# Kernel optimization log

Measured on AMD Instinct MI355X. Metric: run time of the kernel, lower is better.

Reference implementation:

```python
import jax, jax.numpy as jnp
import numpy as np

D_MODEL = 1024
N_HEADS = 16
HEAD = D_MODEL // N_HEADS  # 64


def setup_inputs() -> dict:
    key = jax.random.key(0)
    ks = jax.random.split(key, 6)
    B, T = 2, 2048
    x = jax.random.normal(ks[0], (B, T, D_MODEL), dtype=jnp.float32)
    s_in = 1.0 / np.sqrt(HEAD)
    # per-head projections: Linear(head_size -> d_model), no bias. Stored as [H, head, d_model].
    Wq = jax.random.normal(ks[1], (N_HEADS, HEAD, D_MODEL), dtype=jnp.float32) * s_in
    Wk = jax.random.normal(ks[2], (N_HEADS, HEAD, D_MODEL), dtype=jnp.float32) * s_in
    Wv = jax.random.normal(ks[3], (N_HEADS, HEAD, D_MODEL), dtype=jnp.float32) * s_in
    # output projection: Linear(H*d_model -> d_model) with bias
    Wo = jax.random.normal(ks[4], (N_HEADS * D_MODEL, D_MODEL), dtype=jnp.float32) / np.sqrt(N_HEADS * D_MODEL)
    bo = jax.random.normal(ks[5], (D_MODEL,), dtype=jnp.float32) * 0.01
    return {"x": x, "Wq": Wq, "Wk": Wk, "Wv": Wv, "Wo": Wo, "bo": bo}


def reference(x, Wq, Wk, Wv, Wo, bo):
    B, T, _ = x.shape
    # split into per-head slices: [B, H, T, head]
    xh = x.reshape(B, T, N_HEADS, HEAD).transpose(0, 2, 1, 3)
    q = jnp.einsum("bhtd,hdm->bhtm", xh, Wq)  # [B,H,T,d_model]
    k = jnp.einsum("bhtd,hdm->bhtm", xh, Wk)
    v = jnp.einsum("bhtd,hdm->bhtm", xh, Wv)
    # scale uses D = head input dim (= HEAD), per the original code
    scores = jnp.einsum("bhtm,bhsm->bhts", q, k) / jnp.sqrt(jnp.asarray(HEAD, x.dtype))
    weights = jax.nn.softmax(scores, axis=-1)
    vb = jnp.einsum("bhts,bhsm->bhtm", weights, v)  # [B,H,T,d_model]
    cat = vb.transpose(0, 2, 1, 3).reshape(B, T, N_HEADS * D_MODEL)
    return cat @ Wo + bo
```

## Files before the change

kernel.cpp:

```cpp
#include <hip/hip_runtime.h>
#include <math.h>

typedef unsigned u32;
typedef unsigned short u16;
typedef __attribute__((ext_vector_type(8))) __bf16 bf16x8;
typedef __attribute__((ext_vector_type(4))) float f32x4;

#define DEVI __device__ __forceinline__

DEVI u16 f2bf(float f) {
    u32 u = __builtin_bit_cast(u32, f);
    u += 0x7fffu + ((u >> 16) & 1u);
    return (u16)(u >> 16);
}

DEVI u32 packbf(float a, float b) {
    u32 ua = __builtin_bit_cast(u32, a) + 0x8000u;
    u32 ub = __builtin_bit_cast(u32, b) + 0x8000u;
    return (ua >> 16) | (ub & 0xffff0000u);
}

DEVI bf16x8 ldsf(const u16* p) { return *(const bf16x8*)p; }

DEVI f32x4 mfma16(bf16x8 a, bf16x8 b, f32x4 c) {
    return __builtin_amdgcn_mfma_f32_16x16x32_bf16(a, b, c, 0, 0, 0);
}

#if __has_builtin(__builtin_amdgcn_exp2f)
DEVI float fexp2(float x) { return __builtin_amdgcn_exp2f(x); }
#else
DEVI float fexp2(float x) { return exp2f(x); }
#endif

__global__ __launch_bounds__(256) void k_pw(const float* __restrict__ x,
                                            const float* __restrict__ Wq, const float* __restrict__ Wk,
                                            const float* __restrict__ Wv, const float* __restrict__ Wo,
                                            u16* __restrict__ xswz, u16* __restrict__ xt2,
                                            u16* __restrict__ mtg, u16* __restrict__ W2) {
    __shared__ __align__(16) char SM[36864];
    const int tid = threadIdx.x;
    const int id = blockIdx.x;
    const int rr = tid >> 2, c16 = (tid & 3) * 16;

    if (id < 272) {
        u16* LA0 = (u16*)SM;
        u16* LB0 = (u16*)(SM + 9216);
        u16* LA1 = (u16*)(SM + 18432);
        u16* LB1 = (u16*)(SM + 27648);
        const int w = tid >> 6, lane = tid & 63, g = lane >> 4, ln = lane & 15;
        f32x4 acc[4] = {};
        float4 pa0[4], pb0[4], pa1[4], pb1[4];

        auto mm = [&](const u16* LAp, const u16* LBp) {
#pragma unroll
            for (int ks = 0; ks < 2; ks++) {
                bf16x8 bb = ldsf(LBp + (w * 16 + ln) * 72 + ks * 32 + g * 8);
#pragma unroll
                for (int mt = 0; mt < 4; mt++) {
                    bf16x8 a = ldsf(LAp + (mt * 16 + ln) * 72 + ks * 32 + g * 8);
                    acc[mt] = mfma16(a, bb, acc[mt]);
                }
            }
        };
        auto bar = [&]() {
            asm volatile("s_waitcnt lgkmcnt(0)" ::: "memory");
            __builtin_amdgcn_s_barrier();
            __builtin_amdgcn_sched_barrier(0);
        };

        if (id >= 256) {
            const int h = id - 256;
            auto loadT = [&](int t, float4* pa, float4* pb) {
                const float4* sa = (const float4*)(Wk + (h * 64 + rr) * 1024 + t * 64 + c16);
                const float4* sb = (const float4*)(Wq + (h * 64 + rr) * 1024 + t * 64 + c16);
#pragma unroll
                for (int j = 0; j < 4; j++) { pa[j] = sa[j]; pb[j] = sb[j]; }
            };
            auto cvtW = [&](u16* LAp, u16* LBp, float4* pa, float4* pb) {
                union { uint4 q[2]; u16 s[16]; } ua, ub;
#pragma unroll
                for (int j = 0; j < 4; j++) {
                    ua.s[j*4+0]=f2bf(pa[j].x); ua.s[j*4+1]=f2bf(pa[j].y); ua.s[j*4+2]=f2bf(pa[j].z); ua.s[j*4+3]=f2bf(pa[j].w);
                    ub.s[j*4+0]=f2bf(pb[j].x); ub.s[j*4+1]=f2bf(pb[j].y); ub.s[j*4+2]=f2bf(pb[j].z); ub.s[j*4+3]=f2bf(pb[j].w);
                }
                *(uint4*)(LAp + rr * 72 + c16) = ua.q[0]; *(uint4*)(LAp + rr * 72 + c16 + 8) = ua.q[1];
                *(uint4*)(LBp + rr * 72 + c16) = ub.q[0]; *(uint4*)(LBp + rr * 72 + c16 + 8) = ub.q[1];
            };
            loadT(0, pa0, pb0);
            cvtW(LA0, LB0, pa0, pb0);
            loadT(1, pa1, pb1);
            bar();
            for (int kb = 0; kb < 16; kb += 2) {
                if (kb + 2 < 16) loadT(kb + 2, pa0, pb0);
                mm(LA0, LB0);
                cvtW(LA1, LB1, pa1, pb1);
                bar();
                if (kb + 3 < 16) loadT(kb + 3, pa1, pb1);
                mm(LA1, LB1);
                if (kb + 2 < 16) cvtW(LA0, LB0, pa0, pb0);
                bar();
            }
#pragma unroll
            for (int mt = 0; mt < 4; mt++)
#pragma unroll
                for (int r = 0; r < 4; r++)
                    mtg[h * 4096 + (mt * 16 + g * 4 + r) * 64 + w * 16 + ln] =
                        f2bf(acc[mt][r] * 0.18033688011112f);
        } else {
            const int h = id >> 4, n0 = (id & 15) * 64;
            auto loadT = [&](int t, float4* pa, float4* pb) {
                const float4* sa = (const float4*)(Wo + (h * 1024 + t * 64 + rr) * 1024 + n0 + c16);
                const float4* sb = (const float4*)(Wv + (h * 64 + rr) * 1024 + t * 64 + c16);
#pragma unroll
                for (int j = 0; j < 4; j++) { pa[j] = sa[j]; pb[j] = sb[j]; }
            };
            auto cvtW = [&](u16* LAp, u16* LBp, float4* pa, float4* pb) {
                union { uint4 q[2]; u16 s[16]; } ub;
#pragma unroll
                for (int j = 0; j < 4; j++) {
                    ub.s[j*4+0]=f2bf(pb[j].x); ub.s[j*4+1]=f2bf(pb[j].y); ub.s[j*4+2]=f2bf(pb[j].z); ub.s[j*4+3]=f2bf(pb[j].w);
                }
                *(uint4*)(LBp + rr * 72 + c16) = ub.q[0]; *(uint4*)(LBp + rr * 72 + c16 + 8) = ub.q[1];
#pragma unroll
                for (int j = 0; j < 4; j++) {
                    LAp[(c16 + j * 4 + 0) * 72 + rr] = f2bf(pa[j].x);
                    LAp[(c16 + j * 4 + 1) * 72 + rr] = f2bf(pa[j].y);
                    LAp[(c16 + j * 4 + 2) * 72 + rr] = f2bf(pa[j].z);
                    LAp[(c16 + j * 4 + 3) * 72 + rr] = f2bf(pa[j].w);
                }
            };
            loadT(0, pa0, pb0);
            cvtW(LA0, LB0, pa0, pb0);
            loadT(1, pa1, pb1);
            bar();
            for (int kb = 0; kb < 16; kb += 2) {
                if (kb + 2 < 16) loadT(kb + 2, pa0, pb0);
                mm(LA0, LB0);
                cvtW(LA1, LB1, pa1, pb1);
                bar();
                if (kb + 3 < 16) loadT(kb + 3, pa1, pb1);
                mm(LA1, LB1);
                if (kb + 2 < 16) cvtW(LA0, LB0, pa0, pb0);
                bar();
            }
            int d = w * 16 + ln;
#pragma unroll
            for (int mt = 0; mt < 4; mt++)
#pragma unroll
                for (int r = 0; r < 4; r++) {
                    int n = n0 + mt * 16 + g * 4 + r;
                    W2[h * 65536 + n * 64 + (((d >> 3) ^ (n & 7)) << 3) + (d & 7)] = f2bf(acc[mt][r]);
                }
        }
    } else {
        const int pid = id - 272;
        const int kt = pid & 31, h = (pid >> 5) & 15, b = pid >> 9, bh = b * 16 + h;
        float* T = (float*)SM;
        int t = kt * 64 + rr;
        const float4* gx = (const float4*)(x + (b * 2048 + t) * 1024 + h * 64 + c16);
        float4 f[4];
#pragma unroll
        for (int j = 0; j < 4; j++) f[j] = gx[j];
#pragma unroll
        for (int j = 0; j < 4; j++) {
            T[rr * 65 + c16 + j * 4 + 0] = f[j].x; T[rr * 65 + c16 + j * 4 + 1] = f[j].y;
            T[rr * 65 + c16 + j * 4 + 2] = f[j].z; T[rr * 65 + c16 + j * 4 + 3] = f[j].w;
        }
        {
            union { uint4 q[2]; u16 s[16]; } u;
#pragma unroll
            for (int j = 0; j < 4; j++) {
                u.s[j * 4 + 0] = f2bf(f[j].x); u.s[j * 4 + 1] = f2bf(f[j].y);
                u.s[j * 4 + 2] = f2bf(f[j].z); u.s[j * 4 + 3] = f2bf(f[j].w);
            }
            u16* dst = xswz + (bh * 2048 + t) * 64;
            int c0 = (tid & 3) * 2, sw = rr & 7;
            *(uint4*)(dst + ((c0 ^ sw) << 3))       = u.q[0];
            *(uint4*)(dst + (((c0 + 1) ^ sw) << 3)) = u.q[1];
        }
        __syncthreads();
        int dd = tid >> 2, t4 = (tid & 3) * 16;
        union { uint2 d2[4]; u16 s[16]; } ou;
#pragma unroll
        for (int j = 0; j < 16; j++) ou.s[j] = f2bf(T[(t4 + j) * 65 + dd]);
        u16* dst = xt2 + bh * 131072 + kt * 4096 + dd * 64;
        const int nt0 = t4 >> 4;
        const int cb = (nt0 >> 1) * 4;
        const int off = (nt0 & 1) * 4;
        const int sw = dd & 7;
#pragma unroll
        for (int g4 = 0; g4 < 4; g4++) {
            int c = cb + g4;
            *(uint2*)(dst + ((c ^ sw) << 3) + off) = ou.d2[g4];
        }
    }
}

__global__ __launch_bounds__(256, 2) void k_attn(const u16* __restrict__ xswz, const u16* __restrict__ xt2,
                                                 const u16* __restrict__ mtg, u16* __restrict__ U2) {
    __shared__ __align__(16) u16 smem[16384];
    u16* KB = smem;

    const int tid = threadIdx.x;
    const int w = tid >> 6, lane = tid & 63, g = lane >> 4, ln = lane & 15, ln7 = lane & 7;
    const int nid = (blockIdx.x & 7) * 64 + (blockIdx.x >> 3);
    const int qt = nid & 15, h = (nid >> 4) & 15, b = nid >> 8, bh = b * 16 + h;
    const u16* xs = xswz + bh * 131072;
    const u16* xv = xt2 + bh * 131072;

    bf16x8 qf[2][2];
    {
        u16* LM  = smem;
        u16* LXQ = smem + 4608;
        {
            int r4 = tid >> 2, c4 = (tid & 3) * 2;
            const uint4* gm = (const uint4*)(mtg + h * 4096 + r4 * 64);
            uint4 m0 = gm[c4], m1 = gm[c4 + 1];
            *(uint4*)(LM + r4 * 72 + c4 * 8)     = m0;
            *(uint4*)(LM + r4 * 72 + c4 * 8 + 8) = m1;
            int r2 = tid >> 1, c2 = (tid & 1) * 4;
            const uint4* gx = (const uint4*)(xs + (qt * 128 + r2) * 64);
            uint4 x0 = gx[c2], x1 = gx[c2 + 1], x2 = gx[c2 + 2], x3 = gx[c2 + 3];
            *(uint4*)(LXQ + r2 * 72 + c2 * 8)      = x0;
            *(uint4*)(LXQ + r2 * 72 + c2 * 8 + 8)  = x1;
            *(uint4*)(LXQ + r2 * 72 + c2 * 8 + 16) = x2;
            *(uint4*)(LXQ + r2 * 72 + c2 * 8 + 24) = x3;
        }
        __syncthreads();
        f32x4 acc[2][4] = {};
#pragma unroll
        for (int qh = 0; qh < 2; qh++) {
            int row = qh * 64 + w * 16 + ln;
#pragma unroll
            for (int ks = 0; ks < 2; ks++) {
                bf16x8 a = ldsf(LXQ + row * 72 + (((ks * 4 + g) ^ ln7) << 3));
#pragma unroll
                for (int nt = 0; nt < 4; nt++) {
                    bf16x8 bb = ldsf(LM + (nt * 16 + ln) * 72 + ks * 32 + g * 8);
                    acc[qh][nt] = mfma16(a, bb, acc[qh][nt]);
                }
            }
        }
        __syncthreads();
#pragma unroll
        for (int qh = 0; qh < 2; qh++) {
            u16* QLw = smem + qh * 4608 + w * 1152;
#pragma unroll
            for (int nt = 0; nt < 4; nt++)
#pragma unroll
                for (int r = 0; r < 4; r++)
                    QLw[(g * 4 + r) * 72 + nt * 16 + ln] = f2bf(acc[qh][nt][r]);
        }
        asm volatile("s_waitcnt lgkmcnt(0)" ::: "memory");
#pragma unroll
        for (int qh = 0; qh < 2; qh++) {
            u16* QLw = smem + qh * 4608 + w * 1152;
            qf[qh][0] = ldsf(QLw + ln * 72 + g * 8);
            qf[qh][1] = ldsf(QLw + ln * 72 + 32 + g * 8);
        }
        __syncthreads();
    }

    {
        const uint4* gk = (const uint4*)xs;
        uint4 k0 = gk[tid], k1 = gk[tid + 256];
        uint4* lk = (uint4*)KB;
        lk[tid] = k0; lk[tid + 256] = k1;
    }
    bf16x8 vfA[2][4], vfB[2][4];
#pragma unroll
    for (int ks = 0; ks < 2; ks++)
#pragma unroll
        for (int dt = 0; dt < 4; dt++)
            vfA[ks][dt] = *(const bf16x8*)(xv + (dt * 16 + ln) * 64 + (((ks * 4 + g) ^ ln7) << 3));
    asm volatile("s_waitcnt lgkmcnt(0)" ::: "memory");
    __builtin_amdgcn_s_barrier();
    __builtin_amdgcn_sched_barrier(0);

    float lrow[2] = {0.f, 0.f};
    f32x4 o[2][4] = {};

    auto step = [&](int kt, bf16x8 (&vcur)[2][4], bf16x8 (&vnxt)[2][4]) {
        const int cur = (kt & 1) << 12;
        const u16* KL = KB + cur;
        uint4 kr0, kr1;
        if (kt + 1 < 32) {
            const uint4* gk = (const uint4*)(xs + (kt + 1) * 4096);
            kr0 = gk[tid]; kr1 = gk[tid + 256];
            const u16* gv = xv + (kt + 1) * 4096;
#pragma unroll
            for (int ks = 0; ks < 2; ks++)
#pragma unroll
                for (int dt = 0; dt < 4; dt++)
                    vnxt[ks][dt] = *(const bf16x8*)(gv + (dt * 16 + ln) * 64 + (((ks * 4 + g) ^ ln7) << 3));
        }

        f32x4 s[2][4] = {};
        __builtin_amdgcn_s_setprio(1);
#pragma unroll
        for (int ks = 0; ks < 2; ks++) {
#pragma unroll
            for (int nt = 0; nt < 4; nt++) {
                bf16x8 a = ldsf(KL + (nt * 16 + ln) * 64 + (((ks * 4 + g) ^ ln7) << 3));
                s[0][nt] = mfma16(a, qf[0][ks], s[0][nt]);
                s[1][nt] = mfma16(a, qf[1][ks], s[1][nt]);
            }
        }
        __builtin_amdgcn_s_setprio(0);

        u32 pk[2][4][2];
#pragma unroll
        for (int qh = 0; qh < 2; qh++) {
            float ts = 0.f;
#pragma unroll
            for (int nt = 0; nt < 4; nt++) {
                float p0 = fexp2(s[qh][nt][0]), p1 = fexp2(s[qh][nt][1]);
                float p2 = fexp2(s[qh][nt][2]), p3 = fexp2(s[qh][nt][3]);
                pk[qh][nt][0] = packbf(p0, p1);
                pk[qh][nt][1] = packbf(p2, p3);
                ts += (p0 + p1) + (p2 + p3);
            }
            lrow[qh] += ts;
        }

        __builtin_amdgcn_s_setprio(1);
#pragma unroll
        for (int ks = 0; ks < 2; ks++) {
            union { u32 u[4]; bf16x8 v; } pf[2];
#pragma unroll
            for (int qh = 0; qh < 2; qh++) {
                pf[qh].u[0] = pk[qh][2 * ks][0];
                pf[qh].u[1] = pk[qh][2 * ks][1];
                pf[qh].u[2] = pk[qh][2 * ks + 1][0];
                pf[qh].u[3] = pk[qh][2 * ks + 1][1];
            }
#pragma unroll
            for (int dt = 0; dt < 4; dt++) {
                o[0][dt] = mfma16(vcur[ks][dt], pf[0].v, o[0][dt]);
                o[1][dt] = mfma16(vcur[ks][dt], pf[1].v, o[1][dt]);
            }
        }
        __builtin_amdgcn_s_setprio(0);

        if (kt + 1 < 32) {
            const int nxt = cur ^ 4096;
            uint4* lk = (uint4*)(KB + nxt);
            lk[tid] = kr0; lk[tid + 256] = kr1;
        }
        asm volatile("s_waitcnt lgkmcnt(0)" ::: "memory");
        __builtin_amdgcn_s_barrier();
        __builtin_amdgcn_sched_barrier(0);
    };

    for (int kt = 0; kt < 32; kt += 2) {
        step(kt, vfA, vfB);
        step(kt + 1, vfB, vfA);
    }

#pragma unroll
    for (int qh = 0; qh < 2; qh++) {
        lrow[qh] += __shfl_xor(lrow[qh], 16, 64);
        lrow[qh] += __shfl_xor(lrow[qh], 32, 64);
        float inv = 1.0f / lrow[qh];
        int t = b * 2048 + qt * 128 + qh * 64 + w * 16 + ln;
#pragma unroll
        for (int dt = 0; dt < 4; dt++) {
            ushort4 vv;
            vv.x = f2bf(o[qh][dt][0] * inv); vv.y = f2bf(o[qh][dt][1] * inv);
            vv.z = f2bf(o[qh][dt][2] * inv); vv.w = f2bf(o[qh][dt][3] * inv);
            int c = dt * 2 + (g >> 1);
            int pos = c ^ (t & 7);
            *(ushort4*)(U2 + h * 262144 + t * 64 + pos * 8 + (g & 1) * 4) = vv;
        }
    }
}

__global__ __launch_bounds__(512) void k_out(const u16* __restrict__ U2, const u16* __restrict__ W2,
                                             const float* __restrict__ bo, float* __restrict__ out) {
    __shared__ __align__(16) u16 SMu[32768];
    const int tid = threadIdx.x;
    const int w = tid >> 6, lane = tid & 63, g = lane >> 4, ln = lane & 15;
    const int nid = (blockIdx.x & 7) * 32 + (blockIdx.x >> 3);
    const int n0 = (nid & 7) * 128, r0 = (nid >> 3) * 128;
    const int wr = (w >> 2) * 64, wc = (w & 3) * 32;
    f32x4 acc[4][2] = {};
    uint4 ar[2], br[2];

    {
        const uint4* ga = (const uint4*)(U2 + r0 * 64);
        const uint4* gb = (const uint4*)(W2 + n0 * 64);
        ar[0] = ga[tid]; ar[1] = ga[tid + 512];
        br[0] = gb[tid]; br[1] = gb[tid + 512];
        ((uint4*)SMu)[tid] = ar[0]; ((uint4*)SMu)[tid + 512] = ar[1];
        ((uint4*)(SMu + 16384))[tid] = br[0]; ((uint4*)(SMu + 16384))[tid + 512] = br[1];
    }
    asm volatile("s_waitcnt lgkmcnt(0)" ::: "memory");
    __builtin_amdgcn_s_barrier();
    __builtin_amdgcn_sched_barrier(0);

    for (int kb = 0; kb < 16; kb++) {
        const int cu = (kb & 1) << 13;
        if (kb + 1 < 16) {
            const uint4* ga = (const uint4*)(U2 + (kb + 1) * 262144 + r0 * 64);
            const uint4* gb = (const uint4*)(W2 + (kb + 1) * 65536 + n0 * 64);
            ar[0] = ga[tid]; ar[1] = ga[tid + 512];
            br[0] = gb[tid]; br[1] = gb[tid + 512];
        }
        const u16* AL = SMu + cu;
        const u16* BL = SMu + 16384 + cu;
#pragma unroll
        for (int ks = 0; ks < 2; ks++) {
            bf16x8 af[4], bfr[2];
#pragma unroll
            for (int mt = 0; mt < 4; mt++) {
                int rr = wr + mt * 16 + ln;
                af[mt] = ldsf(AL + rr * 64 + (((ks * 4 + g) ^ (rr & 7)) << 3));
            }
#pragma unroll
            for (int nt = 0; nt < 2; nt++) {
                int rr = wc + nt * 16 + ln;
                bfr[nt] = ldsf(BL + rr * 64 + (((ks * 4 + g) ^ (rr & 7)) << 3));
            }
#pragma unroll
            for (int mt = 0; mt < 4; mt++)
#pragma unroll
                for (int nt = 0; nt < 2; nt++)
                    acc[mt][nt] = mfma16(af[mt], bfr[nt], acc[mt][nt]);
        }
        if (kb + 1 < 16) {
            const int nx = cu ^ 8192;
            uint4* la = (uint4*)(SMu + nx);
            uint4* lb = (uint4*)(SMu + 16384 + nx);
            la[tid] = ar[0]; la[tid + 512] = ar[1];
            lb[tid] = br[0]; lb[tid + 512] = br[1];
        }
        asm volatile("s_waitcnt lgkmcnt(0)" ::: "memory");
        __builtin_amdgcn_s_barrier();
        __builtin_amdgcn_sched_barrier(0);
    }

    float* Wp = (float*)SMu + w * 576;
    const int coff = (lane & 7) * 4;
    const float4 b4 = *(const float4*)(bo + n0 + wc + coff);
#pragma unroll
    for (int mt = 0; mt < 4; mt++) {
#pragma unroll
        for (int nt = 0; nt < 2; nt++)
#pragma unroll
            for (int r = 0; r < 4; r++)
                Wp[(g * 4 + r) * 36 + nt * 16 + ln] = acc[mt][nt][r];
        asm volatile("s_waitcnt lgkmcnt(0)" ::: "memory");
#pragma unroll
        for (int i = 0; i < 2; i++) {
            int row = (lane >> 3) + 8 * i;
            float4 v = *(const float4*)(Wp + row * 36 + coff);
            v.x += b4.x; v.y += b4.y; v.z += b4.z; v.w += b4.w;
            *(float4*)(out + (r0 + wr + mt * 16 + row) * 1024 + n0 + wc + coff) = v;
        }
    }
}

extern "C" void kernel_launch(void* const* d_in, const int* in_sizes, int n_in,
                              void* d_out, int out_size, void* d_ws, size_t ws_size,
                              hipStream_t stream) {
    const float* x  = (const float*)d_in[0];
    const float* Wq = (const float*)d_in[1];
    const float* Wk = (const float*)d_in[2];
    const float* Wv = (const float*)d_in[3];
    const float* Wo = (const float*)d_in[4];
    const float* bo = (const float*)d_in[5];
    float* out = (float*)d_out;

    char* ws = (char*)d_ws;
    u16* xswz = (u16*)(ws);
    u16* mtg  = (u16*)(ws + 8388608);
    u16* xt2  = (u16*)(ws + 8519680);
    u16* W2   = (u16*)(ws + 16908288);
    u16* U2   = (u16*)(ws + 19005440);

    k_pw<<<1296, 256, 0, stream>>>(x, Wq, Wk, Wv, Wo, xswz, xt2, mtg, W2);
    k_attn<<<512, 256, 0, stream>>>(xswz, xt2, mtg, U2);
    k_out<<<256, 512, 0, stream>>>(U2, W2, bo, out);
}
```

Before: 207.8 us.

## Split KV tiles across waves and stage V in LDS with cross-wave reduction

Restructures the attention kernel so each wave handles 64 queries (4 q-tiles) against half of each 64-key tile, instead of 32 queries against the full tile. V is now double-buffered through LDS alongside K rather than loaded per-lane straight from global into registers. At the end, partial outputs and row sums from the two KV-half waves are combined through LDS before normalisation. The aim is more reuse of each K/V fragment across query tiles and coalesced V loads, at the cost of more accumulator registers, extra LDS, and a final reduction pass.

```diff
diff --git a/kernel.cpp b/kernel.cpp
--- a/kernel.cpp
+++ b/kernel.cpp
@@ -198,17 +198,19 @@
 
 __global__ __launch_bounds__(256, 2) void k_attn(const u16* __restrict__ xswz, const u16* __restrict__ xt2,
                                                  const u16* __restrict__ mtg, u16* __restrict__ U2) {
-    __shared__ __align__(16) u16 smem[16384];
+    __shared__ __align__(16) u16 smem[20480];
     u16* KB = smem;
+    u16* VB = smem + 8192;
 
     const int tid = threadIdx.x;
     const int w = tid >> 6, lane = tid & 63, g = lane >> 4, ln = lane & 15, ln7 = lane & 7;
+    const int kvh = w & 1, qh2 = w >> 1;
     const int nid = (blockIdx.x & 7) * 64 + (blockIdx.x >> 3);
-    const int qt = nid & 15, h = (nid >> 4) & 15, b = nid >> 8, bh = b * 16 + h;
+    const int qtb = nid & 15, h = (nid >> 4) & 15, b = nid >> 8, bh = b * 16 + h;
     const u16* xs = xswz + bh * 131072;
     const u16* xv = xt2 + bh * 131072;
 
-    bf16x8 qf[2][2];
+    bf16x8 qf[4][2];
     {
         u16* LM  = smem;
         u16* LXQ = smem + 4608;
@@ -219,7 +221,7 @@
             *(uint4*)(LM + r4 * 72 + c4 * 8)     = m0;
             *(uint4*)(LM + r4 * 72 + c4 * 8 + 8) = m1;
             int r2 = tid >> 1, c2 = (tid & 1) * 4;
-            const uint4* gx = (const uint4*)(xs + (qt * 128 + r2) * 64);
+            const uint4* gx = (const uint4*)(xs + (qtb * 128 + r2) * 64);
             uint4 x0 = gx[c2], x1 = gx[c2 + 1], x2 = gx[c2 + 2], x3 = gx[c2 + 3];
             *(uint4*)(LXQ + r2 * 72 + c2 * 8)      = x0;
             *(uint4*)(LXQ + r2 * 72 + c2 * 8 + 8)  = x1;
@@ -251,48 +253,42 @@
                 for (int r = 0; r < 4; r++)
                     QLw[(g * 4 + r) * 72 + nt * 16 + ln] = f2bf(acc[qh][nt][r]);
         }
-        asm volatile("s_waitcnt lgkmcnt(0)" ::: "memory");
-#pragma unroll
-        for (int qh = 0; qh < 2; qh++) {
-            u16* QLw = smem + qh * 4608 + w * 1152;
-            qf[qh][0] = ldsf(QLw + ln * 72 + g * 8);
-            qf[qh][1] = ldsf(QLw + ln * 72 + 32 + g * 8);
+        __syncthreads();
+#pragma unroll
+        for (int qt = 0; qt < 4; qt++) {
+            const u16* QLr = smem + qh2 * 4608 + qt * 1152;
+            qf[qt][0] = ldsf(QLr + ln * 72 + g * 8);
+            qf[qt][1] = ldsf(QLr + ln * 72 + 32 + g * 8);
         }
         __syncthreads();
     }
 
     {
         const uint4* gk = (const uint4*)xs;
-        uint4 k0 = gk[tid], k1 = gk[tid + 256];
+        const uint4* gv = (const uint4*)xv;
+        uint4 k0 = gk[tid], k1 = gk[tid + 256], v0 = gv[tid], v1 = gv[tid + 256];
         uint4* lk = (uint4*)KB;
-        lk[tid] = k0; lk[tid + 256] = k1;
-    }
-    bf16x8 vfA[2][4], vfB[2][4];
-#pragma unroll
-    for (int ks = 0; ks < 2; ks++)
-#pragma unroll
-        for (int dt = 0; dt < 4; dt++)
-            vfA[ks][dt] = *(const bf16x8*)(xv + (dt * 16 + ln) * 64 + (((ks * 4 + g) ^ ln7) << 3));
+        uint4* lv = (uint4*)VB;
+        lk[tid] = k0; lk[tid + 256] = k1; lv[tid] = v0; lv[tid + 256] = v1;
+    }
     asm volatile("s_waitcnt lgkmcnt(0)" ::: "memory");
     __builtin_amdgcn_s_barrier();
     __builtin_amdgcn_sched_barrier(0);
 
-    float lrow[2] = {0.f, 0.f};
-    f32x4 o[2][4] = {};
-
-    auto step = [&](int kt, bf16x8 (&vcur)[2][4], bf16x8 (&vnxt)[2][4]) {
+    float lrow[4] = {0.f, 0.f, 0.f, 0.f};
+    f32x4 o[4][4] = {};
+
+#pragma unroll 2
+    for (int kt = 0; kt < 32; ++kt) {
         const int cur = (kt & 1) << 12;
         const u16* KL = KB + cur;
-        uint4 kr0, kr1;
+        const u16* VL = VB + cur;
+
+        uint4 kr0, kr1, vr0, vr1;
         if (kt + 1 < 32) {
             const uint4* gk = (const uint4*)(xs + (kt + 1) * 4096);
-            kr0 = gk[tid]; kr1 = gk[tid + 256];
-            const u16* gv = xv + (kt + 1) * 4096;
-#pragma unroll
-            for (int ks = 0; ks < 2; ks++)
-#pragma unroll
-                for (int dt = 0; dt < 4; dt++)
-                    vnxt[ks][dt] = *(const bf16x8*)(gv + (dt * 16 + ln) * 64 + (((ks * 4 + g) ^ ln7) << 3));
+            const uint4* gv = (const uint4*)(xv + (kt + 1) * 4096);
+            kr0 = gk[tid]; kr1 = gk[tid + 256]; vr0 = gv[tid]; vr1 = gv[tid + 256];
         }
 
         f32x4 s[2][4] = {};
@@ -300,44 +296,46 @@
 #pragma unroll
         for (int ks = 0; ks < 2; ks++) {
 #pragma unroll
-            for (int nt = 0; nt < 4; nt++) {
-                bf16x8 a = ldsf(KL + (nt * 16 + ln) * 64 + (((ks * 4 + g) ^ ln7) << 3));
-                s[0][nt] = mfma16(a, qf[0][ks], s[0][nt]);
-                s[1][nt] = mfma16(a, qf[1][ks], s[1][nt]);
+            for (int nt = 0; nt < 2; nt++) {
+                bf16x8 a = ldsf(KL + ((kvh * 2 + nt) * 16 + ln) * 64 + (((ks * 4 + g) ^ ln7) << 3));
+#pragma unroll
+                for (int qt = 0; qt < 4; qt++)
+                    s[nt][qt] = mfma16(a, qf[qt][ks], s[nt][qt]);
             }
         }
         __builtin_amdgcn_s_setprio(0);
 
         u32 pk[2][4][2];
 #pragma unroll
-        for (int qh = 0; qh < 2; qh++) {
+        for (int qt = 0; qt < 4; qt++) {
             float ts = 0.f;
 #pragma unroll
-            for (int nt = 0; nt < 4; nt++) {
-                float p0 = fexp2(s[qh][nt][0]), p1 = fexp2(s[qh][nt][1]);
-                float p2 = fexp2(s[qh][nt][2]), p3 = fexp2(s[qh][nt][3]);
-                pk[qh][nt][0] = packbf(p0, p1);
-                pk[qh][nt][1] = packbf(p2, p3);
+            for (int nt = 0; nt < 2; nt++) {
+                float p0 = fexp2(s[nt][qt][0]), p1 = fexp2(s[nt][qt][1]);
+                float p2 = fexp2(s[nt][qt][2]), p3 = fexp2(s[nt][qt][3]);
+                pk[nt][qt][0] = packbf(p0, p1);
+                pk[nt][qt][1] = packbf(p2, p3);
                 ts += (p0 + p1) + (p2 + p3);
             }
-            lrow[qh] += ts;
+            lrow[qt] += ts;
         }
 
         __builtin_amdgcn_s_setprio(1);
-#pragma unroll
-        for (int ks = 0; ks < 2; ks++) {
-            union { u32 u[4]; bf16x8 v; } pf[2];
-#pragma unroll
-            for (int qh = 0; qh < 2; qh++) {
-                pf[qh].u[0] = pk[qh][2 * ks][0];
-                pf[qh].u[1] = pk[qh][2 * ks][1];
-                pf[qh].u[2] = pk[qh][2 * ks + 1][0];
-                pf[qh].u[3] = pk[qh][2 * ks + 1][1];
+        {
+            union { u32 u[4]; bf16x8 v; } pf[4];
+#pragma unroll
+            for (int qt = 0; qt < 4; qt++) {
+                pf[qt].u[0] = pk[0][qt][0];
+                pf[qt].u[1] = pk[0][qt][1];
+                pf[qt].u[2] = pk[1][qt][0];
+                pf[qt].u[3] = pk[1][qt][1];
             }
 #pragma unroll
             for (int dt = 0; dt < 4; dt++) {
-                o[0][dt] = mfma16(vcur[ks][dt], pf[0].v, o[0][dt]);
-                o[1][dt] = mfma16(vcur[ks][dt], pf[1].v, o[1][dt]);
+                bf16x8 a = ldsf(VL + (dt * 16 + ln) * 64 + (((kvh * 4 + g) ^ ln7) << 3));
+#pragma unroll
+                for (int qt = 0; qt < 4; qt++)
+                    o[dt][qt] = mfma16(a, pf[qt].v, o[dt][qt]);
             }
         }
         __builtin_amdgcn_s_setprio(0);
@@ -345,32 +343,59 @@
         if (kt + 1 < 32) {
             const int nxt = cur ^ 4096;
             uint4* lk = (uint4*)(KB + nxt);
-            lk[tid] = kr0; lk[tid + 256] = kr1;
+            uint4* lv = (uint4*)(VB + nxt);
+            lk[tid] = kr0; lk[tid + 256] = kr1; lv[tid] = vr0; lv[tid + 256] = vr1;
         }
         asm volatile("s_waitcnt lgkmcnt(0)" ::: "memory");
         __builtin_amdgcn_s_barrier();
         __builtin_amdgcn_sched_barrier(0);
-    };
-
-    for (int kt = 0; kt < 32; kt += 2) {
-        step(kt, vfA, vfB);
-        step(kt + 1, vfB, vfA);
-    }
-
-#pragma unroll
-    for (int qh = 0; qh < 2; qh++) {
-        lrow[qh] += __shfl_xor(lrow[qh], 16, 64);
-        lrow[qh] += __shfl_xor(lrow[qh], 32, 64);
-        float inv = 1.0f / lrow[qh];
-        int t = b * 2048 + qt * 128 + qh * 64 + w * 16 + ln;
-#pragma unroll
-        for (int dt = 0; dt < 4; dt++) {
-            ushort4 vv;
-            vv.x = f2bf(o[qh][dt][0] * inv); vv.y = f2bf(o[qh][dt][1] * inv);
-            vv.z = f2bf(o[qh][dt][2] * inv); vv.w = f2bf(o[qh][dt][3] * inv);
-            int c = dt * 2 + (g >> 1);
-            int pos = c ^ (t & 7);
-            *(ushort4*)(U2 + h * 262144 + t * 64 + pos * 8 + (g & 1) * 4) = vv;
+    }
+
+#pragma unroll
+    for (int qt = 0; qt < 4; qt++) {
+        lrow[qt] += __shfl_xor(lrow[qt], 16, 64);
+        lrow[qt] += __shfl_xor(lrow[qt], 32, 64);
+    }
+    float* LO = (float*)smem;
+    if (kvh == 1) {
+        float* B = LO + qh2 * 4290;
+#pragma unroll
+        for (int dt = 0; dt < 4; dt++)
+#pragma unroll
+            for (int qt = 0; qt < 4; qt++)
+#pragma unroll
+                for (int r = 0; r < 4; r++)
+                    B[(dt * 16 + g * 4 + r) * 66 + qt * 16 + ln] = o[dt][qt][r];
+        if (g == 0) {
+#pragma unroll
+            for (int qt = 0; qt < 4; qt++)
+                B[64 * 66 + qt * 16 + ln] = lrow[qt];
+        }
+    }
+    __syncthreads();
+    if (kvh == 0) {
+        float* B = LO + qh2 * 4290;
+#pragma unroll
+        for (int dt = 0; dt < 4; dt++)
+#pragma unroll
+            for (int qt = 0; qt < 4; qt++)
+#pragma unroll
+                for (int r = 0; r < 4; r++)
+                    o[dt][qt][r] += B[(dt * 16 + g * 4 + r) * 66 + qt * 16 + ln];
+#pragma unroll
+        for (int qt = 0; qt < 4; qt++) {
+            float lr = lrow[qt] + B[64 * 66 + qt * 16 + ln];
+            float inv = 1.0f / lr;
+            int t = b * 2048 + qtb * 128 + qh2 * 64 + qt * 16 + ln;
+#pragma unroll
+            for (int dt = 0; dt < 4; dt++) {
+                ushort4 vv;
+                vv.x = f2bf(o[dt][qt][0] * inv); vv.y = f2bf(o[dt][qt][1] * inv);
+                vv.z = f2bf(o[dt][qt][2] * inv); vv.w = f2bf(o[dt][qt][3] * inv);
+                int c = dt * 2 + (g >> 1);
+                int pos = c ^ (t & 7);
+                *(ushort4*)(U2 + h * 262144 + t * 64 + pos * 8 + (g & 1) * 4) = vv;
+            }
         }
     }
 }
```

After: 200.0 us. 1.04x faster.
